# Optimization experiments

Hardware: AMD Instinct MI355X
Metric: run time of the kernel (lower is better)

## Reference

```python
import jax, jax.numpy as jnp
import numpy as np

B, S, D, DM, H, DH, DF, L, T = 4096, 64, 256, 512, 4, 64, 512, 6, 20


def mish(x):
    return x * jnp.tanh(jax.nn.softplus(x))


def layernorm(x, eps=1e-5):
    mu = jnp.mean(x, axis=-1, keepdims=True)
    var = jnp.var(x, axis=-1, keepdims=True)
    return (x - mu) * jax.lax.rsqrt(var + eps)


def setup_inputs() -> dict:
    key = jax.random.key(0)
    ks = iter(jax.random.split(key, 32))
    w = lambda *shape: jax.random.normal(next(ks), shape, dtype=jnp.float32) * 0.02
    inp = {
        'x_t': jax.random.normal(next(ks), (B, S, D), dtype=jnp.float32),
        't': jax.random.randint(next(ks), (B,), 0, T + 1),
        'backbone_latent': jax.random.normal(next(ks), (B, S, DM), dtype=jnp.float32),
        # timestep embedding
        'emb': w(T + 1, D),
        'te_w1': w(D, 4 * D), 'te_b1': jnp.zeros((4 * D,), jnp.float32),
        'te_w2': w(4 * D, D), 'te_b2': jnp.zeros((D,), jnp.float32),
        # cond projection
        'cp_w1': w(DM, D), 'cp_b1': jnp.zeros((D,), jnp.float32),
        'cp_w2': w(D, D), 'cp_b2': jnp.zeros((D,), jnp.float32),
        # stacked per-layer DiT block params [L, ...]
        'adaln_w': w(L, D, 6 * D), 'adaln_b': jnp.zeros((L, 6 * D), jnp.float32),
        'qkv_w': w(L, D, 3 * D), 'qkv_b': jnp.zeros((L, 3 * D), jnp.float32),
        'op_w': w(L, D, D), 'op_b': jnp.zeros((L, D), jnp.float32),
        'ffn_w1': w(L, D, DF), 'ffn_b1': jnp.zeros((L, DF), jnp.float32),
        'ffn_w2': w(L, DF, D), 'ffn_b2': jnp.zeros((L, D), jnp.float32),
        # final adaLN + projection (random here for nontrivial test, zero-init in original)
        'fa_w': w(D, 2 * D), 'fa_b': jnp.zeros((2 * D,), jnp.float32),
        'fp_w': w(D, D), 'fp_b': jnp.zeros((D,), jnp.float32),
    }
    return inp


def _forward(x_t, t, backbone_latent, emb, te_w1, te_b1, te_w2, te_b2,
             cp_w1, cp_b1, cp_w2, cp_b2, adaln_w, adaln_b, qkv_w, qkv_b,
             op_w, op_b, ffn_w1, ffn_b1, ffn_w2, ffn_b2, fa_w, fa_b, fp_w, fp_b):
    # conditioning vector c: [B, D]
    te = emb[t]                                   # [B, D]
    te = mish(te @ te_w1 + te_b1) @ te_w2 + te_b2
    cond = jnp.mean(backbone_latent, axis=1)      # [B, DM]
    cond = mish(cond @ cp_w1 + cp_b1) @ cp_w2 + cp_b2
    c = te + cond
    mc = mish(c)

    x = x_t
    for l in range(L):
        mod = (mc @ adaln_w[l] + adaln_b[l])[:, None, :]   # [B, 1, 6D]
        sh1, sc1, g1, sh2, sc2, g2 = jnp.split(mod, 6, axis=-1)
        # attention sub-block
        h = layernorm(x) * (1.0 + sc1) + sh1
        qkv = (h @ qkv_w[l] + qkv_b[l]).reshape(B, S, 3, H, DH)
        q = qkv[:, :, 0].transpose(0, 2, 1, 3)   # [B, H, S, DH]
        k = qkv[:, :, 1].transpose(0, 2, 1, 3)
        v = qkv[:, :, 2].transpose(0, 2, 1, 3)
        attn = jax.nn.softmax(jnp.einsum('bhsd,bhtd->bhst', q, k) * DH ** -0.5, axis=-1)
        h = jnp.einsum('bhst,bhtd->bhsd', attn, v).transpose(0, 2, 1, 3).reshape(B, S, D)
        h = h @ op_w[l] + op_b[l]
        x = x + g1 * h
        # FFN sub-block
        h = layernorm(x) * (1.0 + sc2) + sh2
        h = mish(h @ ffn_w1[l] + ffn_b1[l]) @ ffn_w2[l] + ffn_b2[l]
        x = x + g2 * h

    mod = (mc @ fa_w + fa_b)[:, None, :]
    shift, scale = jnp.split(mod, 2, axis=-1)
    x = layernorm(x) * (1.0 + scale) + shift
    return x @ fp_w + fp_b


def reference(x_t, t, backbone_latent, emb, te_w1, te_b1, te_w2, te_b2,
              cp_w1, cp_b1, cp_w2, cp_b2, adaln_w, adaln_b, qkv_w, qkv_b,
              op_w, op_b, ffn_w1, ffn_b1, ffn_w2, ffn_b2, fa_w, fa_b, fp_w, fp_b):
    return _forward(x_t, t, backbone_latent, emb, te_w1, te_b1, te_w2, te_b2,
                    cp_w1, cp_b1, cp_w2, cp_b2, adaln_w, adaln_b, qkv_w, qkv_b,
                    op_w, op_b, ffn_w1, ffn_b1, ffn_w2, ffn_b2, fa_w, fa_b, fp_w, fp_b)
```

## Files before the change

### kernel.cpp

```cpp
#include <hip/hip_runtime.h>

typedef unsigned short u16;
typedef float f32x4 __attribute__((ext_vector_type(4)));
typedef __bf16 bf16x8 __attribute__((ext_vector_type(8)));

__device__ __forceinline__ u16 f2b(float f) {
  unsigned u = __builtin_bit_cast(unsigned, f);
  u += 0x7FFF + ((u >> 16) & 1);
  return (u16)(u >> 16);
}

__device__ __forceinline__ float mishf(float x) {
  float e = __expf(fminf(x, 20.f));
  float n = e * (e + 2.f);
  return x * __fdividef(n, n + 2.f);
}

__device__ __forceinline__ void gl_lds16(const void* g, void* l) {
  __builtin_amdgcn_global_load_lds((__attribute__((address_space(1))) void*)g,
                                   (__attribute__((address_space(3))) void*)l, 16, 0, 0);
}

__device__ __forceinline__ bf16x8 ldb8(const u16* p) {
  return __builtin_bit_cast(bf16x8, *(const uint4*)p);
}

__global__ __launch_bounds__(256)
void transpose_w(const float* __restrict__ in, u16* __restrict__ out, int K, int N) {
  __shared__ float tl[64][65];
  const long zoff = (long)blockIdx.z * K * N;
  in += zoff; out += zoff;
  const int n0 = blockIdx.x * 64, k0 = blockIdx.y * 64;
  const int c = threadIdx.x & 63, r0 = threadIdx.x >> 6;
#pragma unroll
  for (int i = 0; i < 16; ++i) {
    int r = i * 4 + r0;
    tl[r][c] = in[(long)(k0 + r) * N + n0 + c];
  }
  __syncthreads();
#pragma unroll
  for (int i = 0; i < 16; ++i) {
    int r = i * 4 + r0;
    out[(long)(n0 + r) * K + k0 + c] = f2b(tl[c][r]);
  }
}

__global__ __launch_bounds__(1024)
void te_table_kernel(const float* __restrict__ emb, const float* __restrict__ w1,
                     const float* __restrict__ b1, const float* __restrict__ w2,
                     const float* __restrict__ b2, float* __restrict__ table) {
  __shared__ float te[256];
  __shared__ float h1[1024];
  __shared__ float red[1024];
  const int tt = blockIdx.x, tid = threadIdx.x;
  if (tid < 256) te[tid] = emb[tt * 256 + tid];
  __syncthreads();
  float a = b1[tid];
#pragma unroll 8
  for (int k = 0; k < 256; ++k) a += te[k] * w1[k * 1024 + tid];
  h1[tid] = mishf(a);
  __syncthreads();
  const int j = tid & 255, kq = tid >> 8;
  float a2 = 0.f;
#pragma unroll 8
  for (int k = kq * 256; k < kq * 256 + 256; ++k) a2 += h1[k] * w2[k * 256 + j];
  red[tid] = a2;
  __syncthreads();
  if (tid < 256)
    table[tt * 256 + tid] = b2[tid] + red[tid] + red[tid + 256] + red[tid + 512] + red[tid + 768];
}

__global__ __launch_bounds__(256)
void cond_mean_kernel(const float* __restrict__ bb, u16* __restrict__ cond) {
  const int b = blockIdx.x, tid = threadIdx.x;
  const float* p = bb + (long)b * 64 * 512;
  for (int d = tid; d < 512; d += 256) {
    float s = 0.f;
#pragma unroll
    for (int t = 0; t < 64; ++t) s += p[t * 512 + d];
    cond[b * 512 + d] = f2b(s * (1.f / 64.f));
  }
}

__global__ __launch_bounds__(256)
void ln_mod(const float* __restrict__ x, const float* __restrict__ modb,
            int mstride, int shoff, int scoff, u16* __restrict__ out) {
  const int lane = threadIdx.x & 63;
  const long row = (long)blockIdx.x * 4 + (threadIdx.x >> 6);
  const float4 xv = *(const float4*)(x + row * 256 + lane * 4);
  float s1 = xv.x + xv.y + xv.z + xv.w;
  float s2 = xv.x * xv.x + xv.y * xv.y + xv.z * xv.z + xv.w * xv.w;
#pragma unroll
  for (int m = 1; m < 64; m <<= 1) { s1 += __shfl_xor(s1, m); s2 += __shfl_xor(s2, m); }
  const float mean = s1 * (1.f / 256.f);
  float var = s2 * (1.f / 256.f) - mean * mean;
  const float rstd = rsqrtf(fmaxf(var, 0.f) + 1e-5f);
  const long b = row >> 6;
  const float4 sc = *(const float4*)(modb + b * mstride + scoff + lane * 4);
  const float4 sh = *(const float4*)(modb + b * mstride + shoff + lane * 4);
  ushort4 o;
  o.x = f2b((xv.x - mean) * rstd * (1.f + sc.x) + sh.x);
  o.y = f2b((xv.y - mean) * rstd * (1.f + sc.y) + sh.y);
  o.z = f2b((xv.z - mean) * rstd * (1.f + sc.z) + sh.z);
  o.w = f2b((xv.w - mean) * rstd * (1.f + sc.w) + sh.w);
  *(ushort4*)(out + row * 256 + lane * 4) = o;
}

template <int EPI>
__global__ __launch_bounds__(256)
void gemm_bt(const u16* __restrict__ A, const u16* __restrict__ Bt,
             const float* __restrict__ bias, void* __restrict__ outp,
             const int* __restrict__ tvec, const float* __restrict__ tetab,
             int M, int N, int K) {
  __shared__ __align__(16) u16 As[128 * 64];
  __shared__ __align__(16) u16 Bs[128 * 64];
  const int tid = threadIdx.x;
  const int lane = tid & 63;
  const int wave = tid >> 6;
  const int wr = (wave >> 1) << 6;
  const int wc = (wave & 1) << 6;
  const long tm = (long)blockIdx.y * 128;
  const long tn = (long)blockIdx.x * 128;
  const u16* Ag = A + tm * K;
  const u16* Bg = Bt + tn * K;
  f32x4 acc[4][4] = {};
  const int kcb = lane >> 4;
  const int swz = lane & 7;
  for (int k0 = 0; k0 < K; k0 += 64) {
#pragma unroll
    for (int i = 0; i < 4; ++i) {
      int c = tid + (i << 8);
      int r = c >> 3;
      int sch = (c & 7) ^ (r & 7);
      gl_lds16(Ag + (long)r * K + k0 + (sch << 3), &As[c << 3]);
    }
#pragma unroll
    for (int i = 0; i < 4; ++i) {
      int c = tid + (i << 8);
      int r = c >> 3;
      int sch = (c & 7) ^ (r & 7);
      gl_lds16(Bg + (long)r * K + k0 + (sch << 3), &Bs[c << 3]);
    }
    __syncthreads();
#pragma unroll
    for (int kt = 0; kt < 2; ++kt) {
      const int ko = ((kt * 4 + kcb) ^ swz) << 3;
      bf16x8 av[4], bv[4];
#pragma unroll
      for (int mt = 0; mt < 4; ++mt)
        av[mt] = ldb8(&As[(wr + mt * 16 + (lane & 15)) * 64 + ko]);
#pragma unroll
      for (int nt = 0; nt < 4; ++nt)
        bv[nt] = ldb8(&Bs[(wc + nt * 16 + (lane & 15)) * 64 + ko]);
#pragma unroll
      for (int mt = 0; mt < 4; ++mt)
#pragma unroll
        for (int nt = 0; nt < 4; ++nt)
          acc[mt][nt] = __builtin_amdgcn_mfma_f32_16x16x32_bf16(bv[nt], av[mt], acc[mt][nt], 0, 0, 0);
    }
    __syncthreads();
  }
  const int rl = lane & 15;
  const int c4 = (lane >> 4) << 2;
  f32x4 b4[4];
#pragma unroll
  for (int nt = 0; nt < 4; ++nt)
    b4[nt] = *(const f32x4*)(bias + (int)tn + wc + nt * 16 + c4);
#pragma unroll
  for (int mt = 0; mt < 4; ++mt) {
    const unsigned row = (unsigned)(tm + wr + mt * 16 + rl);
    const unsigned rb = row * (unsigned)N;
#pragma unroll
    for (int nt = 0; nt < 4; ++nt) {
      const unsigned col = (unsigned)tn + wc + nt * 16 + c4;
      f32x4 v = acc[mt][nt] + b4[nt];
      if constexpr (EPI == 0) {
        ushort4 o;
        o.x = f2b(v[0]); o.y = f2b(v[1]); o.z = f2b(v[2]); o.w = f2b(v[3]);
        *(ushort4*)((u16*)outp + rb + col) = o;
      } else if constexpr (EPI == 1) {
        ushort4 o;
        o.x = f2b(mishf(v[0])); o.y = f2b(mishf(v[1]));
        o.z = f2b(mishf(v[2])); o.w = f2b(mishf(v[3]));
        *(ushort4*)((u16*)outp + rb + col) = o;
      } else if constexpr (EPI == 3) {
        *(f32x4*)((float*)outp + rb + col) = v;
      } else {
        const f32x4 te = *(const f32x4*)(tetab + tvec[row] * 256 + col);
        ushort4 o;
        o.x = f2b(mishf(v[0] + te[0])); o.y = f2b(mishf(v[1] + te[1]));
        o.z = f2b(mishf(v[2] + te[2])); o.w = f2b(mishf(v[3] + te[3]));
        *(ushort4*)((u16*)outp + rb + col) = o;
      }
    }
  }
}

__global__ __launch_bounds__(512)
void gemm_ln(const u16* __restrict__ A, const u16* __restrict__ Bt,
             const float* __restrict__ bias, const float* __restrict__ xin,
             const float* __restrict__ gptr,
             const float* __restrict__ lnsh, const float* __restrict__ lnsc, int lnstride,
             float* __restrict__ xout, u16* __restrict__ hout, int K) {
  __shared__ __align__(16) u16 As[128 * 64];
  __shared__ __align__(16) u16 Bs[256 * 64];
  const int tid = threadIdx.x, lane = tid & 63, wave = tid >> 6;
  const int wr = wave * 16;
  const long tm = (long)blockIdx.x * 128;
  const u16* Ag = A + tm * K;
  f32x4 acc[16] = {};
  const int kcb = lane >> 4, swz = lane & 7;
  for (int k0 = 0; k0 < K; k0 += 64) {
#pragma unroll
    for (int i = 0; i < 2; ++i) {
      int c = tid + (i << 9);
      int r = c >> 3;
      int sch = (c & 7) ^ (r & 7);
      gl_lds16(Ag + (long)r * K + k0 + (sch << 3), &As[c << 3]);
    }
#pragma unroll
    for (int i = 0; i < 4; ++i) {
      int c = tid + (i << 9);
      int r = c >> 3;
      int sch = (c & 7) ^ (r & 7);
      gl_lds16(Bt + (long)r * K + k0 + (sch << 3), &Bs[c << 3]);
    }
    __syncthreads();
#pragma unroll
    for (int kt = 0; kt < 2; ++kt) {
      const int ko = ((kt * 4 + kcb) ^ swz) << 3;
      bf16x8 av = ldb8(&As[(wr + (lane & 15)) * 64 + ko]);
#pragma unroll
      for (int nt = 0; nt < 16; ++nt) {
        bf16x8 bv = ldb8(&Bs[(nt * 16 + (lane & 15)) * 64 + ko]);
        acc[nt] = __builtin_amdgcn_mfma_f32_16x16x32_bf16(bv, av, acc[nt], 0, 0, 0);
      }
    }
    __syncthreads();
  }
  const int rl = lane & 15;
  const int c4 = (lane >> 4) << 2;
  const long row = tm + wr + rl;
  const long b = (tm + wr) >> 6;
  float s1 = 0.f, s2 = 0.f;
#pragma unroll
  for (int nt = 0; nt < 16; ++nt) {
    const int col = nt * 16 + c4;
    const f32x4 b4 = *(const f32x4*)(bias + col);
    const f32x4 g4 = *(const f32x4*)(gptr + b * 1536 + col);
    const f32x4 x = *(const f32x4*)(xin + row * 256 + col);
    f32x4 xn = x + g4 * (acc[nt] + b4);
    acc[nt] = xn;
    s1 += xn[0] + xn[1] + xn[2] + xn[3];
    s2 += xn[0] * xn[0] + xn[1] * xn[1] + xn[2] * xn[2] + xn[3] * xn[3];
  }
  s1 += __shfl_xor(s1, 16); s1 += __shfl_xor(s1, 32);
  s2 += __shfl_xor(s2, 16); s2 += __shfl_xor(s2, 32);
  const float mean = s1 * (1.f / 256.f);
  const float var = s2 * (1.f / 256.f) - mean * mean;
  const float rstd = rsqrtf(fmaxf(var, 0.f) + 1e-5f);
#pragma unroll
  for (int nt = 0; nt < 16; ++nt) {
    const int col = nt * 16 + c4;
    const f32x4 sc4 = *(const f32x4*)(lnsc + b * lnstride + col);
    const f32x4 sh4 = *(const f32x4*)(lnsh + b * lnstride + col);
    *(f32x4*)(xout + row * 256 + col) = acc[nt];
    f32x4 h = (acc[nt] - mean) * rstd * (1.f + sc4) + sh4;
    ushort4 o;
    o.x = f2b(h[0]); o.y = f2b(h[1]); o.z = f2b(h[2]); o.w = f2b(h[3]);
    *(ushort4*)(hout + row * 256 + col) = o;
  }
}

__global__ __launch_bounds__(128)
void attn_kernel(const u16* __restrict__ qkv, u16* __restrict__ out) {
  __shared__ __align__(16) u16 vt_s[2][64 * 72];
  __shared__ __align__(16) u16 p_s[2][64 * 72];
  const int lane = threadIdx.x & 63;
  const int wave = threadIdx.x >> 6;
  const long b = blockIdx.x >> 1;
  const int h = ((blockIdx.x & 1) << 1) | wave;
  u16* vt = vt_s[wave];
  u16* pl = p_s[wave];
  const u16* base = qkv + b * (64 * 768);
#pragma unroll
  for (int it = 0; it < 8; ++it) {
    int chunk = it * 64 + lane;
    int t = chunk >> 3, dhb = (chunk & 7) << 3;
    union { uint4 u; u16 s[8]; } uv;
    uv.u = *(const uint4*)(base + t * 768 + 512 + h * 64 + dhb);
#pragma unroll
    for (int j = 0; j < 8; ++j) vt[(dhb + j) * 72 + t] = uv.s[j];
  }
  const u16* qb = base + h * 64;
  const u16* kb = base + 256 + h * 64;
  f32x4 sacc[4][4] = {};
#pragma unroll
  for (int kt = 0; kt < 2; ++kt) {
    bf16x8 qa[4], kv[4];
#pragma unroll
    for (int mt = 0; mt < 4; ++mt)
      qa[mt] = ldb8(qb + ((lane & 15) + mt * 16) * 768 + kt * 32 + ((lane >> 4) << 3));
#pragma unroll
    for (int nt = 0; nt < 4; ++nt)
      kv[nt] = ldb8(kb + ((lane & 15) + nt * 16) * 768 + kt * 32 + ((lane >> 4) << 3));
#pragma unroll
    for (int mt = 0; mt < 4; ++mt)
#pragma unroll
      for (int nt = 0; nt < 4; ++nt)
        sacc[mt][nt] = __builtin_amdgcn_mfma_f32_16x16x32_bf16(qa[mt], kv[nt], sacc[mt][nt], 0, 0, 0);
  }
  const float scale = 0.125f;
#pragma unroll
  for (int mt = 0; mt < 4; ++mt) {
#pragma unroll
    for (int r = 0; r < 4; ++r) {
      float mx = fmaxf(fmaxf(sacc[mt][0][r], sacc[mt][1][r]), fmaxf(sacc[mt][2][r], sacc[mt][3][r]));
#pragma unroll
      for (int m = 1; m <= 8; m <<= 1) mx = fmaxf(mx, __shfl_xor(mx, m));
      float p[4];
      float sum = 0.f;
#pragma unroll
      for (int nt = 0; nt < 4; ++nt) { p[nt] = __expf((sacc[mt][nt][r] - mx) * scale); sum += p[nt]; }
#pragma unroll
      for (int m = 1; m <= 8; m <<= 1) sum += __shfl_xor(sum, m);
      const float rinv = 1.f / sum;
      const int s = mt * 16 + ((lane >> 4) << 2) + r;
#pragma unroll
      for (int nt = 0; nt < 4; ++nt) pl[s * 72 + nt * 16 + (lane & 15)] = f2b(p[nt] * rinv);
    }
  }
  __syncthreads();
  f32x4 oacc[4][4] = {};
#pragma unroll
  for (int kt = 0; kt < 2; ++kt) {
    bf16x8 pa[4], vv[4];
#pragma unroll
    for (int mt = 0; mt < 4; ++mt)
      pa[mt] = ldb8(pl + ((lane & 15) + mt * 16) * 72 + kt * 32 + ((lane >> 4) << 3));
#pragma unroll
    for (int nt = 0; nt < 4; ++nt)
      vv[nt] = ldb8(vt + ((lane & 15) + nt * 16) * 72 + kt * 32 + ((lane >> 4) << 3));
#pragma unroll
    for (int mt = 0; mt < 4; ++mt)
#pragma unroll
      for (int nt = 0; nt < 4; ++nt)
        oacc[mt][nt] = __builtin_amdgcn_mfma_f32_16x16x32_bf16(vv[nt], pa[mt], oacc[mt][nt], 0, 0, 0);
  }
  u16* ob = out + b * (64 * 256) + h * 64;
#pragma unroll
  for (int mt = 0; mt < 4; ++mt)
#pragma unroll
    for (int nt = 0; nt < 4; ++nt) {
      const int s = mt * 16 + (lane & 15);
      const int d4 = nt * 16 + ((lane >> 4) << 2);
      ushort4 o;
      o.x = f2b(oacc[mt][nt][0]); o.y = f2b(oacc[mt][nt][1]);
      o.z = f2b(oacc[mt][nt][2]); o.w = f2b(oacc[mt][nt][3]);
      *(ushort4*)(ob + s * 256 + d4) = o;
    }
}

extern "C" void kernel_launch(void* const* d_in, const int* in_sizes, int n_in,
                              void* d_out, int out_size, void* d_ws, size_t ws_size,
                              hipStream_t stream) {
  (void)in_sizes; (void)n_in; (void)out_size; (void)ws_size;
  const int B = 4096, L = 6;
  const long BSr = (long)B * 64;

  const float* x_t = (const float*)d_in[0];
  const int* tvec = (const int*)d_in[1];
  const float* backbone = (const float*)d_in[2];
  const float* emb = (const float*)d_in[3];
  const float* te_w1 = (const float*)d_in[4];
  const float* te_b1 = (const float*)d_in[5];
  const float* te_w2 = (const float*)d_in[6];
  const float* te_b2 = (const float*)d_in[7];
  const float* cp_w1 = (const float*)d_in[8];
  const float* cp_b1 = (const float*)d_in[9];
  const float* cp_w2 = (const float*)d_in[10];
  const float* cp_b2 = (const float*)d_in[11];
  const float* adaln_w = (const float*)d_in[12];
  const float* adaln_b = (const float*)d_in[13];
  const float* qkv_w = (const float*)d_in[14];
  const float* qkv_b = (const float*)d_in[15];
  const float* op_w = (const float*)d_in[16];
  const float* op_b = (const float*)d_in[17];
  const float* ffn_w1 = (const float*)d_in[18];
  const float* ffn_b1 = (const float*)d_in[19];
  const float* ffn_w2 = (const float*)d_in[20];
  const float* ffn_b2 = (const float*)d_in[21];
  const float* fa_w = (const float*)d_in[22];
  const float* fa_b = (const float*)d_in[23];
  const float* fp_w = (const float*)d_in[24];
  const float* fp_b = (const float*)d_in[25];

  char* w = (char*)d_ws;
  auto alloc = [&](size_t bytes) { char* p = w; w += (bytes + 255) & ~(size_t)255; return p; };
  u16* WT_cp1 = (u16*)alloc(256L * 512 * 2);
  u16* WT_cp2 = (u16*)alloc(256L * 256 * 2);
  u16* WT_adaln = (u16*)alloc(6L * 1536 * 256 * 2);
  u16* WT_qkv = (u16*)alloc(6L * 768 * 256 * 2);
  u16* WT_op = (u16*)alloc(6L * 256 * 256 * 2);
  u16* WT_f1 = (u16*)alloc(6L * 512 * 256 * 2);
  u16* WT_f2 = (u16*)alloc(6L * 256 * 512 * 2);
  u16* WT_fa = (u16*)alloc(512L * 256 * 2);
  u16* WT_fp = (u16*)alloc(256L * 256 * 2);
  float* te_tab = (float*)alloc(21L * 256 * 4);
  u16* cond = (u16*)alloc(4096L * 512 * 2);
  u16* c1 = (u16*)alloc(4096L * 256 * 2);
  u16* mc = (u16*)alloc(4096L * 256 * 2);
  float* modb6 = (float*)alloc(6L * 4096 * 1536 * 4);
  float* famod = (float*)alloc(4096L * 512 * 4);
  u16* hbuf = (u16*)alloc(BSr * 256 * 2);
  u16* qkvbuf = (u16*)alloc(BSr * 768 * 2);
  float* xbuf = (float*)d_out;

  transpose_w<<<dim3(4, 8, 1), 256, 0, stream>>>(cp_w1, WT_cp1, 512, 256);
  transpose_w<<<dim3(4, 4, 1), 256, 0, stream>>>(cp_w2, WT_cp2, 256, 256);
  transpose_w<<<dim3(24, 4, 6), 256, 0, stream>>>(adaln_w, WT_adaln, 256, 1536);
  transpose_w<<<dim3(12, 4, 6), 256, 0, stream>>>(qkv_w, WT_qkv, 256, 768);
  transpose_w<<<dim3(4, 4, 6), 256, 0, stream>>>(op_w, WT_op, 256, 256);
  transpose_w<<<dim3(8, 4, 6), 256, 0, stream>>>(ffn_w1, WT_f1, 256, 512);
  transpose_w<<<dim3(4, 8, 6), 256, 0, stream>>>(ffn_w2, WT_f2, 512, 256);
  transpose_w<<<dim3(8, 4, 1), 256, 0, stream>>>(fa_w, WT_fa, 256, 512);
  transpose_w<<<dim3(4, 4, 1), 256, 0, stream>>>(fp_w, WT_fp, 256, 256);

  te_table_kernel<<<21, 1024, 0, stream>>>(emb, te_w1, te_b1, te_w2, te_b2, te_tab);
  cond_mean_kernel<<<4096, 256, 0, stream>>>(backbone, cond);

  gemm_bt<1><<<dim3(2, 32), 256, 0, stream>>>(cond, WT_cp1, cp_b1, c1, nullptr, nullptr, 4096, 256, 512);
  gemm_bt<4><<<dim3(2, 32), 256, 0, stream>>>(c1, WT_cp2, cp_b2, mc, tvec, te_tab, 4096, 256, 256);
  gemm_bt<3><<<dim3(4, 32), 256, 0, stream>>>(mc, WT_fa, fa_b, famod, nullptr, nullptr, 4096, 512, 256);
  for (int l = 0; l < L; ++l)
    gemm_bt<3><<<dim3(12, 32), 256, 0, stream>>>(mc, WT_adaln + (long)l * 1536 * 256, adaln_b + l * 1536,
                                                 modb6 + (long)l * 4096 * 1536, nullptr, nullptr, 4096, 1536, 256);

  ln_mod<<<BSr / 4, 256, 0, stream>>>(x_t, modb6, 1536, 0, 256, hbuf);

  for (int l = 0; l < L; ++l) {
    const float* mb = modb6 + (long)l * 4096 * 1536;
    gemm_bt<0><<<dim3(6, BSr / 128), 256, 0, stream>>>(hbuf, WT_qkv + (long)l * 768 * 256, qkv_b + l * 768,
                                                       qkvbuf, nullptr, nullptr, (int)BSr, 768, 256);
    attn_kernel<<<B * 2, 128, 0, stream>>>(qkvbuf, hbuf);
    gemm_ln<<<BSr / 128, 512, 0, stream>>>(hbuf, WT_op + (long)l * 256 * 256, op_b + l * 256,
                                           (l == 0) ? x_t : xbuf, mb + 512,
                                           mb + 768, mb + 1024, 1536, xbuf, hbuf, 256);
    gemm_bt<1><<<dim3(4, BSr / 128), 256, 0, stream>>>(hbuf, WT_f1 + (long)l * 512 * 256, ffn_b1 + l * 512,
                                                       qkvbuf, nullptr, nullptr, (int)BSr, 512, 256);
    const float* nsh = (l < 5) ? (modb6 + (long)(l + 1) * 4096 * 1536) : famod;
    const float* nsc = (l < 5) ? (modb6 + (long)(l + 1) * 4096 * 1536 + 256) : (famod + 256);
    const int nstride = (l < 5) ? 1536 : 512;
    gemm_ln<<<BSr / 128, 512, 0, stream>>>(qkvbuf, WT_f2 + (long)l * 256 * 512, ffn_b2 + l * 256,
                                           xbuf, mb + 1280, nsh, nsc, nstride, xbuf, hbuf, 512);
  }
  gemm_bt<3><<<dim3(2, BSr / 128), 256, 0, stream>>>(hbuf, WT_fp, fp_b, d_out, nullptr, nullptr, (int)BSr, 256, 256);
}
```

Baseline: 7.311 ms.

## Double-buffer LDS tiles in GEMMs and shrink gemm_ln to 64-row blocks

Both GEMM kernels now keep two LDS buffers and issue the global-to-LDS loads for the next K tile before computing on the current one. This overlaps memory latency with MFMA work and removes one barrier per iteration. gemm_ln also drops to 64-row tiles with 256 threads, doubling the grid, and the batch index is simplified to blockIdx.x. The cost is double the LDS footprint per block, which may reduce occupancy, and the full 256-column B tile is now reloaded by twice as many blocks.

```diff
diff --git a/kernel.cpp b/kernel.cpp
--- a/kernel.cpp
+++ b/kernel.cpp
@@ -112,8 +112,8 @@
              const float* __restrict__ bias, void* __restrict__ outp,
              const int* __restrict__ tvec, const float* __restrict__ tetab,
              int M, int N, int K) {
-  __shared__ __align__(16) u16 As[128 * 64];
-  __shared__ __align__(16) u16 Bs[128 * 64];
+  __shared__ __align__(16) u16 As[2][128 * 64];
+  __shared__ __align__(16) u16 Bs[2][128 * 64];
   const int tid = threadIdx.x;
   const int lane = tid & 63;
   const int wave = tid >> 6;
@@ -126,32 +126,41 @@
   f32x4 acc[4][4] = {};
   const int kcb = lane >> 4;
   const int swz = lane & 7;
-  for (int k0 = 0; k0 < K; k0 += 64) {
+  const int NT = K >> 6;
+
+  auto stage = [&](int t, int buf) {
+    const int k0 = t << 6;
 #pragma unroll
     for (int i = 0; i < 4; ++i) {
       int c = tid + (i << 8);
       int r = c >> 3;
       int sch = (c & 7) ^ (r & 7);
-      gl_lds16(Ag + (long)r * K + k0 + (sch << 3), &As[c << 3]);
+      gl_lds16(Ag + (long)r * K + k0 + (sch << 3), &As[buf][c << 3]);
     }
 #pragma unroll
     for (int i = 0; i < 4; ++i) {
       int c = tid + (i << 8);
       int r = c >> 3;
       int sch = (c & 7) ^ (r & 7);
-      gl_lds16(Bg + (long)r * K + k0 + (sch << 3), &Bs[c << 3]);
-    }
-    __syncthreads();
+      gl_lds16(Bg + (long)r * K + k0 + (sch << 3), &Bs[buf][c << 3]);
+    }
+  };
+
+  stage(0, 0);
+  __syncthreads();
+  int cur = 0;
+  for (int t = 0; t < NT; ++t) {
+    if (t + 1 < NT) stage(t + 1, cur ^ 1);
 #pragma unroll
     for (int kt = 0; kt < 2; ++kt) {
       const int ko = ((kt * 4 + kcb) ^ swz) << 3;
       bf16x8 av[4], bv[4];
 #pragma unroll
       for (int mt = 0; mt < 4; ++mt)
-        av[mt] = ldb8(&As[(wr + mt * 16 + (lane & 15)) * 64 + ko]);
+        av[mt] = ldb8(&As[cur][(wr + mt * 16 + (lane & 15)) * 64 + ko]);
 #pragma unroll
       for (int nt = 0; nt < 4; ++nt)
-        bv[nt] = ldb8(&Bs[(wc + nt * 16 + (lane & 15)) * 64 + ko]);
+        bv[nt] = ldb8(&Bs[cur][(wc + nt * 16 + (lane & 15)) * 64 + ko]);
 #pragma unroll
       for (int mt = 0; mt < 4; ++mt)
 #pragma unroll
@@ -159,6 +168,7 @@
           acc[mt][nt] = __builtin_amdgcn_mfma_f32_16x16x32_bf16(bv[nt], av[mt], acc[mt][nt], 0, 0, 0);
     }
     __syncthreads();
+    cur ^= 1;
   }
   const int rl = lane & 15;
   const int c4 = (lane >> 4) << 2;
@@ -196,52 +206,62 @@
   }
 }
 
-__global__ __launch_bounds__(512)
+__global__ __launch_bounds__(256)
 void gemm_ln(const u16* __restrict__ A, const u16* __restrict__ Bt,
              const float* __restrict__ bias, const float* __restrict__ xin,
              const float* __restrict__ gptr,
              const float* __restrict__ lnsh, const float* __restrict__ lnsc, int lnstride,
              float* __restrict__ xout, u16* __restrict__ hout, int K) {
-  __shared__ __align__(16) u16 As[128 * 64];
-  __shared__ __align__(16) u16 Bs[256 * 64];
+  __shared__ __align__(16) u16 As[2][64 * 64];
+  __shared__ __align__(16) u16 Bs[2][256 * 64];
   const int tid = threadIdx.x, lane = tid & 63, wave = tid >> 6;
   const int wr = wave * 16;
-  const long tm = (long)blockIdx.x * 128;
+  const long tm = (long)blockIdx.x * 64;
   const u16* Ag = A + tm * K;
   f32x4 acc[16] = {};
   const int kcb = lane >> 4, swz = lane & 7;
-  for (int k0 = 0; k0 < K; k0 += 64) {
+  const int NT = K >> 6;
+
+  auto stage = [&](int t, int buf) {
+    const int k0 = t << 6;
 #pragma unroll
     for (int i = 0; i < 2; ++i) {
-      int c = tid + (i << 9);
+      int c = tid + (i << 8);
       int r = c >> 3;
       int sch = (c & 7) ^ (r & 7);
-      gl_lds16(Ag + (long)r * K + k0 + (sch << 3), &As[c << 3]);
-    }
-#pragma unroll
-    for (int i = 0; i < 4; ++i) {
-      int c = tid + (i << 9);
+      gl_lds16(Ag + (long)r * K + k0 + (sch << 3), &As[buf][c << 3]);
+    }
+#pragma unroll
+    for (int i = 0; i < 8; ++i) {
+      int c = tid + (i << 8);
       int r = c >> 3;
       int sch = (c & 7) ^ (r & 7);
-      gl_lds16(Bt + (long)r * K + k0 + (sch << 3), &Bs[c << 3]);
-    }
-    __syncthreads();
+      gl_lds16(Bt + (long)r * K + k0 + (sch << 3), &Bs[buf][c << 3]);
+    }
+  };
+
+  stage(0, 0);
+  __syncthreads();
+  int cur = 0;
+  for (int t = 0; t < NT; ++t) {
+    if (t + 1 < NT) stage(t + 1, cur ^ 1);
 #pragma unroll
     for (int kt = 0; kt < 2; ++kt) {
       const int ko = ((kt * 4 + kcb) ^ swz) << 3;
-      bf16x8 av = ldb8(&As[(wr + (lane & 15)) * 64 + ko]);
+      bf16x8 av = ldb8(&As[cur][(wr + (lane & 15)) * 64 + ko]);
 #pragma unroll
       for (int nt = 0; nt < 16; ++nt) {
-        bf16x8 bv = ldb8(&Bs[(nt * 16 + (lane & 15)) * 64 + ko]);
+        bf16x8 bv = ldb8(&Bs[cur][(nt * 16 + (lane & 15)) * 64 + ko]);
         acc[nt] = __builtin_amdgcn_mfma_f32_16x16x32_bf16(bv, av, acc[nt], 0, 0, 0);
       }
     }
     __syncthreads();
+    cur ^= 1;
   }
   const int rl = lane & 15;
   const int c4 = (lane >> 4) << 2;
   const long row = tm + wr + rl;
-  const long b = (tm + wr) >> 6;
+  const long b = blockIdx.x;
   float s1 = 0.f, s2 = 0.f;
 #pragma unroll
   for (int nt = 0; nt < 16; ++nt) {
@@ -443,16 +463,16 @@
     gemm_bt<0><<<dim3(6, BSr / 128), 256, 0, stream>>>(hbuf, WT_qkv + (long)l * 768 * 256, qkv_b + l * 768,
                                                        qkvbuf, nullptr, nullptr, (int)BSr, 768, 256);
     attn_kernel<<<B * 2, 128, 0, stream>>>(qkvbuf, hbuf);
-    gemm_ln<<<BSr / 128, 512, 0, stream>>>(hbuf, WT_op + (long)l * 256 * 256, op_b + l * 256,
-                                           (l == 0) ? x_t : xbuf, mb + 512,
-                                           mb + 768, mb + 1024, 1536, xbuf, hbuf, 256);
+    gemm_ln<<<BSr / 64, 256, 0, stream>>>(hbuf, WT_op + (long)l * 256 * 256, op_b + l * 256,
+                                          (l == 0) ? x_t : xbuf, mb + 512,
+                                          mb + 768, mb + 1024, 1536, xbuf, hbuf, 256);
     gemm_bt<1><<<dim3(4, BSr / 128), 256, 0, stream>>>(hbuf, WT_f1 + (long)l * 512 * 256, ffn_b1 + l * 512,
                                                        qkvbuf, nullptr, nullptr, (int)BSr, 512, 256);
     const float* nsh = (l < 5) ? (modb6 + (long)(l + 1) * 4096 * 1536) : famod;
     const float* nsc = (l < 5) ? (modb6 + (long)(l + 1) * 4096 * 1536 + 256) : (famod + 256);
     const int nstride = (l < 5) ? 1536 : 512;
-    gemm_ln<<<BSr / 128, 512, 0, stream>>>(qkvbuf, WT_f2 + (long)l * 256 * 512, ffn_b2 + l * 256,
-                                           xbuf, mb + 1280, nsh, nsc, nstride, xbuf, hbuf, 512);
+    gemm_ln<<<BSr / 64, 256, 0, stream>>>(qkvbuf, WT_f2 + (long)l * 256 * 512, ffn_b2 + l * 256,
+                                          xbuf, mb + 1280, nsh, nsc, nstride, xbuf, hbuf, 512);
   }
   gemm_bt<3><<<dim3(2, BSr / 128), 256, 0, stream>>>(hbuf, WT_fp, fp_b, d_out, nullptr, nullptr, (int)BSr, 256, 256);
 }
```

New measurement: 7.059 ms. -3.4%, faster.

## Drop LDS staging in GEMMs; load MFMA operands directly from global

Applied to the files above, without the earlier changes.

Both GEMM kernels stop staging A/B tiles through shared memory with async global-to-LDS loads and barriers. Instead each lane reads its bf16x8 MFMA fragments straight from global memory, relying on L1/L2 for reuse, with K made a template parameter so the loop fully unrolls. gemm_ln is also reshaped from 512 threads with 128-row tiles to 256 threads with 64-row tiles (one batch per block). This removes barrier and LDS traffic, but adds redundant global and cache traffic and uncoalesced 16-byte reads across waves, especially for the full 256-wide B operand in gemm_ln.

```diff
diff --git a/kernel.cpp b/kernel.cpp
--- a/kernel.cpp
+++ b/kernel.cpp
@@ -14,11 +14,6 @@
   float e = __expf(fminf(x, 20.f));
   float n = e * (e + 2.f);
   return x * __fdividef(n, n + 2.f);
-}
-
-__device__ __forceinline__ void gl_lds16(const void* g, void* l) {
-  __builtin_amdgcn_global_load_lds((__attribute__((address_space(1))) void*)g,
-                                   (__attribute__((address_space(3))) void*)l, 16, 0, 0);
 }
 
 __device__ __forceinline__ bf16x8 ldb8(const u16* p) {
@@ -106,14 +101,11 @@
   *(ushort4*)(out + row * 256 + lane * 4) = o;
 }
 
-template <int EPI>
+template <int EPI, int K>
 __global__ __launch_bounds__(256)
 void gemm_bt(const u16* __restrict__ A, const u16* __restrict__ Bt,
              const float* __restrict__ bias, void* __restrict__ outp,
-             const int* __restrict__ tvec, const float* __restrict__ tetab,
-             int M, int N, int K) {
-  __shared__ __align__(16) u16 As[128 * 64];
-  __shared__ __align__(16) u16 Bs[128 * 64];
+             const int* __restrict__ tvec, const float* __restrict__ tetab, int N) {
   const int tid = threadIdx.x;
   const int lane = tid & 63;
   const int wave = tid >> 6;
@@ -121,46 +113,28 @@
   const int wc = (wave & 1) << 6;
   const long tm = (long)blockIdx.y * 128;
   const long tn = (long)blockIdx.x * 128;
-  const u16* Ag = A + tm * K;
-  const u16* Bg = Bt + tn * K;
+  const int rl = lane & 15;
+  const int kcb = (lane >> 4) << 3;
+  const u16* Ar[4];
+  const u16* Br[4];
+#pragma unroll
+  for (int mt = 0; mt < 4; ++mt) Ar[mt] = A + (tm + wr + mt * 16 + rl) * K + kcb;
+#pragma unroll
+  for (int nt = 0; nt < 4; ++nt) Br[nt] = Bt + (tn + wc + nt * 16 + rl) * K + kcb;
   f32x4 acc[4][4] = {};
-  const int kcb = lane >> 4;
-  const int swz = lane & 7;
-  for (int k0 = 0; k0 < K; k0 += 64) {
-#pragma unroll
-    for (int i = 0; i < 4; ++i) {
-      int c = tid + (i << 8);
-      int r = c >> 3;
-      int sch = (c & 7) ^ (r & 7);
-      gl_lds16(Ag + (long)r * K + k0 + (sch << 3), &As[c << 3]);
-    }
-#pragma unroll
-    for (int i = 0; i < 4; ++i) {
-      int c = tid + (i << 8);
-      int r = c >> 3;
-      int sch = (c & 7) ^ (r & 7);
-      gl_lds16(Bg + (long)r * K + k0 + (sch << 3), &Bs[c << 3]);
-    }
-    __syncthreads();
-#pragma unroll
-    for (int kt = 0; kt < 2; ++kt) {
-      const int ko = ((kt * 4 + kcb) ^ swz) << 3;
-      bf16x8 av[4], bv[4];
-#pragma unroll
-      for (int mt = 0; mt < 4; ++mt)
-        av[mt] = ldb8(&As[(wr + mt * 16 + (lane & 15)) * 64 + ko]);
+#pragma unroll
+  for (int k = 0; k < K; k += 32) {
+    bf16x8 av[4], bv[4];
+#pragma unroll
+    for (int mt = 0; mt < 4; ++mt) av[mt] = ldb8(Ar[mt] + k);
+#pragma unroll
+    for (int nt = 0; nt < 4; ++nt) bv[nt] = ldb8(Br[nt] + k);
+#pragma unroll
+    for (int mt = 0; mt < 4; ++mt)
 #pragma unroll
       for (int nt = 0; nt < 4; ++nt)
-        bv[nt] = ldb8(&Bs[(wc + nt * 16 + (lane & 15)) * 64 + ko]);
-#pragma unroll
-      for (int mt = 0; mt < 4; ++mt)
-#pragma unroll
-        for (int nt = 0; nt < 4; ++nt)
-          acc[mt][nt] = __builtin_amdgcn_mfma_f32_16x16x32_bf16(bv[nt], av[mt], acc[mt][nt], 0, 0, 0);
-    }
-    __syncthreads();
-  }
-  const int rl = lane & 15;
+        acc[mt][nt] = __builtin_amdgcn_mfma_f32_16x16x32_bf16(bv[nt], av[mt], acc[mt][nt], 0, 0, 0);
+  }
   const int c4 = (lane >> 4) << 2;
   f32x4 b4[4];
 #pragma unroll
@@ -196,52 +170,33 @@
   }
 }
 
-__global__ __launch_bounds__(512)
+template <int K>
+__global__ __launch_bounds__(256)
 void gemm_ln(const u16* __restrict__ A, const u16* __restrict__ Bt,
              const float* __restrict__ bias, const float* __restrict__ xin,
              const float* __restrict__ gptr,
              const float* __restrict__ lnsh, const float* __restrict__ lnsc, int lnstride,
-             float* __restrict__ xout, u16* __restrict__ hout, int K) {
-  __shared__ __align__(16) u16 As[128 * 64];
-  __shared__ __align__(16) u16 Bs[256 * 64];
+             float* __restrict__ xout, u16* __restrict__ hout) {
   const int tid = threadIdx.x, lane = tid & 63, wave = tid >> 6;
   const int wr = wave * 16;
-  const long tm = (long)blockIdx.x * 128;
-  const u16* Ag = A + tm * K;
+  const long tm = (long)blockIdx.x * 64;
+  const int rl = lane & 15;
+  const int kcb = (lane >> 4) << 3;
+  const u16* Ar = A + (tm + wr + rl) * K + kcb;
+  const u16* Brb = Bt + (long)rl * K + kcb;
   f32x4 acc[16] = {};
-  const int kcb = lane >> 4, swz = lane & 7;
-  for (int k0 = 0; k0 < K; k0 += 64) {
-#pragma unroll
-    for (int i = 0; i < 2; ++i) {
-      int c = tid + (i << 9);
-      int r = c >> 3;
-      int sch = (c & 7) ^ (r & 7);
-      gl_lds16(Ag + (long)r * K + k0 + (sch << 3), &As[c << 3]);
+#pragma unroll
+  for (int k = 0; k < K; k += 32) {
+    const bf16x8 av = ldb8(Ar + k);
+#pragma unroll
+    for (int nt = 0; nt < 16; ++nt) {
+      bf16x8 bv = ldb8(Brb + (long)nt * 16 * K + k);
+      acc[nt] = __builtin_amdgcn_mfma_f32_16x16x32_bf16(bv, av, acc[nt], 0, 0, 0);
     }
-#pragma unroll
-    for (int i = 0; i < 4; ++i) {
-      int c = tid + (i << 9);
-      int r = c >> 3;
-      int sch = (c & 7) ^ (r & 7);
-      gl_lds16(Bt + (long)r * K + k0 + (sch << 3), &Bs[c << 3]);
-    }
-    __syncthreads();
-#pragma unroll
-    for (int kt = 0; kt < 2; ++kt) {
-      const int ko = ((kt * 4 + kcb) ^ swz) << 3;
-      bf16x8 av = ldb8(&As[(wr + (lane & 15)) * 64 + ko]);
-#pragma unroll
-      for (int nt = 0; nt < 16; ++nt) {
-        bf16x8 bv = ldb8(&Bs[(nt * 16 + (lane & 15)) * 64 + ko]);
-        acc[nt] = __builtin_amdgcn_mfma_f32_16x16x32_bf16(bv, av, acc[nt], 0, 0, 0);
-      }
-    }
-    __syncthreads();
-  }
-  const int rl = lane & 15;
+  }
   const int c4 = (lane >> 4) << 2;
   const long row = tm + wr + rl;
-  const long b = (tm + wr) >> 6;
+  const long b = blockIdx.x;
   float s1 = 0.f, s2 = 0.f;
 #pragma unroll
   for (int nt = 0; nt < 16; ++nt) {
@@ -429,30 +384,30 @@
   te_table_kernel<<<21, 1024, 0, stream>>>(emb, te_w1, te_b1, te_w2, te_b2, te_tab);
   cond_mean_kernel<<<4096, 256, 0, stream>>>(backbone, cond);
 
-  gemm_bt<1><<<dim3(2, 32), 256, 0, stream>>>(cond, WT_cp1, cp_b1, c1, nullptr, nullptr, 4096, 256, 512);
-  gemm_bt<4><<<dim3(2, 32), 256, 0, stream>>>(c1, WT_cp2, cp_b2, mc, tvec, te_tab, 4096, 256, 256);
-  gemm_bt<3><<<dim3(4, 32), 256, 0, stream>>>(mc, WT_fa, fa_b, famod, nullptr, nullptr, 4096, 512, 256);
+  gemm_bt<1, 512><<<dim3(2, 32), 256, 0, stream>>>(cond, WT_cp1, cp_b1, c1, nullptr, nullptr, 256);
+  gemm_bt<4, 256><<<dim3(2, 32), 256, 0, stream>>>(c1, WT_cp2, cp_b2, mc, tvec, te_tab, 256);
+  gemm_bt<3, 256><<<dim3(4, 32), 256, 0, stream>>>(mc, WT_fa, fa_b, famod, nullptr, nullptr, 512);
   for (int l = 0; l < L; ++l)
-    gemm_bt<3><<<dim3(12, 32), 256, 0, stream>>>(mc, WT_adaln + (long)l * 1536 * 256, adaln_b + l * 1536,
-                                                 modb6 + (long)l * 4096 * 1536, nullptr, nullptr, 4096, 1536, 256);
+    gemm_bt<3, 256><<<dim3(12, 32), 256, 0, stream>>>(mc, WT_adaln + (long)l * 1536 * 256, adaln_b + l * 1536,
+                                                      modb6 + (long)l * 4096 * 1536, nullptr, nullptr, 1536);
 
   ln_mod<<<BSr / 4, 256, 0, stream>>>(x_t, modb6, 1536, 0, 256, hbuf);
 
   for (int l = 0; l < L; ++l) {
     const float* mb = modb6 + (long)l * 4096 * 1536;
-    gemm_bt<0><<<dim3(6, BSr / 128), 256, 0, stream>>>(hbuf, WT_qkv + (long)l * 768 * 256, qkv_b + l * 768,
-                                                       qkvbuf, nullptr, nullptr, (int)BSr, 768, 256);
+    gemm_bt<0, 256><<<dim3(6, BSr / 128), 256, 0, stream>>>(hbuf, WT_qkv + (long)l * 768 * 256, qkv_b + l * 768,
+                                                            qkvbuf, nullptr, nullptr, 768);
     attn_kernel<<<B * 2, 128, 0, stream>>>(qkvbuf, hbuf);
-    gemm_ln<<<BSr / 128, 512, 0, stream>>>(hbuf, WT_op + (long)l * 256 * 256, op_b + l * 256,
-                                           (l == 0) ? x_t : xbuf, mb + 512,
-                                           mb + 768, mb + 1024, 1536, xbuf, hbuf, 256);
-    gemm_bt<1><<<dim3(4, BSr / 128), 256, 0, stream>>>(hbuf, WT_f1 + (long)l * 512 * 256, ffn_b1 + l * 512,
-                                                       qkvbuf, nullptr, nullptr, (int)BSr, 512, 256);
+    gemm_ln<256><<<BSr / 64, 256, 0, stream>>>(hbuf, WT_op + (long)l * 256 * 256, op_b + l * 256,
+                                               (l == 0) ? x_t : xbuf, mb + 512,
+                                               mb + 768, mb + 1024, 1536, xbuf, hbuf);
+    gemm_bt<1, 256><<<dim3(4, BSr / 128), 256, 0, stream>>>(hbuf, WT_f1 + (long)l * 512 * 256, ffn_b1 + l * 512,
+                                                            qkvbuf, nullptr, nullptr, 512);
     const float* nsh = (l < 5) ? (modb6 + (long)(l + 1) * 4096 * 1536) : famod;
     const float* nsc = (l < 5) ? (modb6 + (long)(l + 1) * 4096 * 1536 + 256) : (famod + 256);
     const int nstride = (l < 5) ? 1536 : 512;
-    gemm_ln<<<BSr / 128, 512, 0, stream>>>(qkvbuf, WT_f2 + (long)l * 256 * 512, ffn_b2 + l * 256,
-                                           xbuf, mb + 1280, nsh, nsc, nstride, xbuf, hbuf, 512);
-  }
-  gemm_bt<3><<<dim3(2, BSr / 128), 256, 0, stream>>>(hbuf, WT_fp, fp_b, d_out, nullptr, nullptr, (int)BSr, 256, 256);
-}
+    gemm_ln<512><<<BSr / 64, 256, 0, stream>>>(qkvbuf, WT_f2 + (long)l * 256 * 512, ffn_b2 + l * 256,
+                                               xbuf, mb + 1280, nsh, nsc, nstride, xbuf, hbuf);
+  }
+  gemm_bt<3, 256><<<dim3(2, BSr / 128), 256, 0, stream>>>(hbuf, WT_fp, fp_b, d_out, nullptr, nullptr, 256);
+}
```

Result: slower. 12.01 ms (+64.3%).
